# Kernel tuning notes

Hardware: AMD Instinct MI355X
Metric: run time of the kernel (lower is better)

## Reference

```python
import jax, jax.numpy as jnp
import numpy as np

B, L, D, H = 2, 1024, 1024, 16
HD = D // H
HIDDEN = 4 * D
EPS = 1e-6
SCALE = HD ** -0.5

# RoPE tables (head_dim is even, so rope_dim == head_dim)
_inv_freq = 1.0 / (10000.0 ** (np.arange(0, HD, 2, dtype=np.float32) / HD))
_freqs = np.arange(L, dtype=np.float32)[:, None] * _inv_freq[None, :]          # [L, HD/2]
COS = jnp.asarray(np.concatenate([np.cos(_freqs), np.cos(_freqs)], -1))        # [L, HD]
SIN = jnp.asarray(np.concatenate([np.sin(_freqs), np.sin(_freqs)], -1))
MASK = jnp.tril(jnp.ones((L, L), dtype=bool))                                   # causal


def _clin(xr, xi, Wr, Wi, br=None, bi=None):
    # complex linear: (a+bi)(c+di), weights stored [out, in] as in torch
    r = xr @ Wr.T - xi @ Wi.T
    i = xr @ Wi.T + xi @ Wr.T
    if br is not None:
        r = r + br
        i = i + bi
    return r, i


def _cln(xr, xi, gr, gi, br, bi):
    mr = xr.mean(-1, keepdims=True)
    mi = xi.mean(-1, keepdims=True)
    cr = xr - mr
    ci = xi - mi
    var = (cr * cr + ci * ci).mean(-1, keepdims=True)
    s = jnp.sqrt(var + EPS)
    nr = cr / s
    ni = ci / s
    return nr * gr - ni * gi + br, nr * gi + ni * gr + bi


def _rot_half(x):
    h = x.shape[-1] // 2
    return jnp.concatenate([-x[..., h:], x[..., :h]], -1)


def _rope(xr, xi):
    # apply same real rotation to real and imag parts (matches torch code)
    return (xr * COS + _rot_half(xr) * SIN, xi * COS + _rot_half(xi) * SIN)


def _split_heads(x):
    return x.reshape(B, L, H, HD).transpose(0, 2, 1, 3)  # [B,H,L,HD]


def _merge_heads(x):
    return x.transpose(0, 2, 1, 3).reshape(B, L, D)


def setup_inputs() -> dict:
    key = jax.random.key(0)
    ks = jax.random.split(key, 20)
    n = lambda k, shape, s=1.0: jax.random.normal(k, shape, dtype=jnp.float32) * s
    s_attn = (2.0 * (D + D)) ** -0.5
    s_fc1 = (2.0 * (D + HIDDEN)) ** -0.5
    s_fc2 = (2.0 * (HIDDEN + D)) ** -0.5
    return {
        'x_real': n(ks[0], (B, L, D)),
        'x_imag': n(ks[1], (B, L, D)),
        'Wq_r': n(ks[2], (D, D), s_attn), 'Wq_i': n(ks[3], (D, D), s_attn),
        'Wk_r': n(ks[4], (D, D), s_attn), 'Wk_i': n(ks[5], (D, D), s_attn),
        'Wv_r': n(ks[6], (D, D), s_attn), 'Wv_i': n(ks[7], (D, D), s_attn),
        'Wo_r': n(ks[8], (D, D), s_attn), 'Wo_i': n(ks[9], (D, D), s_attn),
        'bo_r': jnp.zeros((D,), jnp.float32), 'bo_i': jnp.zeros((D,), jnp.float32),
        'ln1_gr': jnp.ones((D,), jnp.float32), 'ln1_gi': jnp.zeros((D,), jnp.float32),
        'ln1_br': jnp.zeros((D,), jnp.float32), 'ln1_bi': jnp.zeros((D,), jnp.float32),
        'ln2_gr': jnp.ones((D,), jnp.float32), 'ln2_gi': jnp.zeros((D,), jnp.float32),
        'ln2_br': jnp.zeros((D,), jnp.float32), 'ln2_bi': jnp.zeros((D,), jnp.float32),
        'W1_r': n(ks[10], (HIDDEN, D), s_fc1), 'W1_i': n(ks[11], (HIDDEN, D), s_fc1),
        'b1_r': jnp.zeros((HIDDEN,), jnp.float32), 'b1_i': jnp.zeros((HIDDEN,), jnp.float32),
        'W2_r': n(ks[12], (D, HIDDEN), s_fc2), 'W2_i': n(ks[13], (D, HIDDEN), s_fc2),
        'b2_r': jnp.zeros((D,), jnp.float32), 'b2_i': jnp.zeros((D,), jnp.float32),
        'mod_b': n(ks[14], (HIDDEN,), 0.1),
    }


def reference(x_real, x_imag,
              Wq_r, Wq_i, Wk_r, Wk_i, Wv_r, Wv_i, Wo_r, Wo_i, bo_r, bo_i,
              ln1_gr, ln1_gi, ln1_br, ln1_bi, ln2_gr, ln2_gi, ln2_br, ln2_bi,
              W1_r, W1_i, b1_r, b1_i, W2_r, W2_i, b2_r, b2_i, mod_b):
    # --- attention sublayer (pre-LN) ---
    hr, hi = _cln(x_real, x_imag, ln1_gr, ln1_gi, ln1_br, ln1_bi)
    Qr, Qi = _clin(hr, hi, Wq_r, Wq_i)
    Kr, Ki = _clin(hr, hi, Wk_r, Wk_i)
    Vr, Vi = _clin(hr, hi, Wv_r, Wv_i)
    Qr, Qi, Kr, Ki = map(_split_heads, (Qr, Qi, Kr, Ki))
    Vr, Vi = _split_heads(Vr), _split_heads(Vi)
    Qr, Qi = _rope(Qr, Qi)
    Kr, Ki = _rope(Kr, Ki)
    # Hermitian inner product real part: Re(Q K*) = Qr.Kr + Qi.Ki
    scores = (jnp.einsum('bhld,bhmd->bhlm', Qr, Kr)
              + jnp.einsum('bhld,bhmd->bhlm', Qi, Ki)) * SCALE
    scores = jnp.where(MASK, scores, -jnp.inf)
    attn = jax.nn.softmax(scores, axis=-1)
    out_r = _merge_heads(jnp.einsum('bhlm,bhmd->bhld', attn, Vr))
    out_i = _merge_heads(jnp.einsum('bhlm,bhmd->bhld', attn, Vi))
    out_r, out_i = _clin(out_r, out_i, Wo_r, Wo_i, bo_r, bo_i)
    ar = x_real + out_r
    ai = x_imag + out_i
    # --- feed-forward sublayer (pre-LN) ---
    hr, hi = _cln(ar, ai, ln2_gr, ln2_gi, ln2_br, ln2_bi)
    fr, fi = _clin(hr, hi, W1_r, W1_i, b1_r, b1_i)
    # ModReLU: relu(|z| + b) * e^{i angle(z)}
    mag = jnp.sqrt(fr * fr + fi * fi)
    safe = jnp.where(mag > 0, mag, 1.0)
    act = jax.nn.relu(mag + mod_b)
    fr, fi = act * fr / safe, act * fi / safe
    fr, fi = _clin(fr, fi, W2_r, W2_i, b2_r, b2_i)
    return ar + fr, ai + fi
```

## Files before the change

### kernel.cpp

```cpp
#include <hip/hip_runtime.h>

#define Bq 2
#define Lq 1024
#define Dq 1024
#define Hq 16
#define HDq 64
#define HIDq 4096
#define Mq (Bq*Lq)

typedef __bf16 bf16x8 __attribute__((ext_vector_type(8)));
typedef float floatx4 __attribute__((ext_vector_type(4)));

__device__ __forceinline__ unsigned short f2us(float f){
  unsigned u = __builtin_bit_cast(unsigned, f);
  u = u + 0x7fffu + ((u >> 16) & 1u);
  return (unsigned short)(u >> 16);
}

__device__ __forceinline__ void gld16(const unsigned short* g, unsigned short* l){
  __builtin_amdgcn_global_load_lds(
      (const __attribute__((address_space(1))) unsigned int*)g,
      (__attribute__((address_space(3))) unsigned int*)l, 16, 0, 0);
}

__global__ __launch_bounds__(256) void cvt4_kernel(
    const float* __restrict__ s0, const float* __restrict__ s1,
    const float* __restrict__ s2, const float* __restrict__ s3,
    unsigned short* __restrict__ d0, unsigned short* __restrict__ d1,
    unsigned short* __restrict__ d2, unsigned short* __restrict__ d3,
    int n)
{
  const int a = blockIdx.y;
  const float* s = (a==0) ? s0 : (a==1) ? s1 : (a==2) ? s2 : s3;
  unsigned short* d = (a==0) ? d0 : (a==1) ? d1 : (a==2) ? d2 : d3;
  const int i = (blockIdx.x * 256 + threadIdx.x) * 8;
  if (i >= n) return;
  float4 v0 = ((const float4*)(s + i))[0];
  float4 v1 = ((const float4*)(s + i))[1];
  ushort4 o0, o1;
  o0.x=f2us(v0.x); o0.y=f2us(v0.y); o0.z=f2us(v0.z); o0.w=f2us(v0.w);
  o1.x=f2us(v1.x); o1.y=f2us(v1.y); o1.z=f2us(v1.z); o1.w=f2us(v1.w);
  ((ushort4*)(d + i))[0] = o0;
  ((ushort4*)(d + i))[1] = o1;
}

__global__ __launch_bounds__(256) void cln_kernel(
    const float* __restrict__ xr, const float* __restrict__ xi,
    const float* __restrict__ gr, const float* __restrict__ gi,
    const float* __restrict__ br, const float* __restrict__ bi,
    unsigned short* __restrict__ outr, unsigned short* __restrict__ outi)
{
  const int row = blockIdx.x;
  const int t = threadIdx.x;
  const int lane = t & 63, wv = t >> 6;
  __shared__ float sred[8];

  float4 v4r = ((const float4*)(xr + (size_t)row*Dq))[t];
  float4 v4i = ((const float4*)(xi + (size_t)row*Dq))[t];
  float vr[4] = {v4r.x, v4r.y, v4r.z, v4r.w};
  float vi[4] = {v4i.x, v4i.y, v4i.z, v4i.w};
  float sr = vr[0]+vr[1]+vr[2]+vr[3];
  float si = vi[0]+vi[1]+vi[2]+vi[3];
  #pragma unroll
  for (int o=32;o>0;o>>=1){ sr += __shfl_down(sr,o,64); si += __shfl_down(si,o,64); }
  if (lane==0){ sred[wv]=sr; sred[4+wv]=si; }
  __syncthreads();
  float mr = (sred[0]+sred[1]+sred[2]+sred[3]) * (1.0f/Dq);
  float mi = (sred[4]+sred[5]+sred[6]+sred[7]) * (1.0f/Dq);
  float cr[4], ci[4], vs = 0.f;
  #pragma unroll
  for (int j=0;j<4;++j){ cr[j]=vr[j]-mr; ci[j]=vi[j]-mi; vs += cr[j]*cr[j]+ci[j]*ci[j]; }
  #pragma unroll
  for (int o=32;o>0;o>>=1) vs += __shfl_down(vs,o,64);
  __syncthreads();
  if (lane==0) sred[wv]=vs;
  __syncthreads();
  float var = (sred[0]+sred[1]+sred[2]+sred[3]) * (1.0f/Dq);
  float inv = rsqrtf(var + 1e-6f);

  float4 g4r = ((const float4*)gr)[t];
  float4 g4i = ((const float4*)gi)[t];
  float4 b4r = ((const float4*)br)[t];
  float4 b4i = ((const float4*)bi)[t];
  float grf[4] = {g4r.x,g4r.y,g4r.z,g4r.w};
  float gif[4] = {g4i.x,g4i.y,g4i.z,g4i.w};
  float brf[4] = {b4r.x,b4r.y,b4r.z,b4r.w};
  float bif[4] = {b4i.x,b4i.y,b4i.z,b4i.w};
  ushort4 o_r, o_i;
  unsigned short orr[4], oii[4];
  #pragma unroll
  for (int j=0;j<4;++j){
    float nr = cr[j]*inv, ni = ci[j]*inv;
    orr[j] = f2us(nr*grf[j] - ni*gif[j] + brf[j]);
    oii[j] = f2us(nr*gif[j] + ni*grf[j] + bif[j]);
  }
  o_r.x=orr[0]; o_r.y=orr[1]; o_r.z=orr[2]; o_r.w=orr[3];
  o_i.x=oii[0]; o_i.y=oii[1]; o_i.z=oii[2]; o_i.w=oii[3];
  ((ushort4*)(outr + (size_t)row*Dq))[t] = o_r;
  ((ushort4*)(outi + (size_t)row*Dq))[t] = o_i;
}

template<int EPI, bool ROPE, bool SPLIT3>
__global__ __launch_bounds__(256,3) void cgemm16_kernel(
    const unsigned short* __restrict__ Ar, const unsigned short* __restrict__ Ai,
    const unsigned short* __restrict__ Wr, const unsigned short* __restrict__ Wi,
    void* __restrict__ Cr0, void* __restrict__ Ci0,
    void* __restrict__ Cr1, void* __restrict__ Ci1,
    void* __restrict__ Cr2, void* __restrict__ Ci2,
    const float* __restrict__ biasR, const float* __restrict__ biasI,
    const float* __restrict__ resR, const float* __restrict__ resI,
    const float* __restrict__ modb,
    int Ndim, int Kdim)
{
  const int t = threadIdx.x;
  const int w = t >> 6, lane = t & 63;
  const int quad = lane >> 4, l15 = lane & 15;
  const int wr = w >> 1, wc = w & 1;
  const int m0 = blockIdx.x * 64, n0 = blockIdx.y * 64;

  __shared__ __align__(16) unsigned short sAr0[64*32], sAi0[64*32], sWr0[64*32], sWi0[64*32];
  __shared__ __align__(16) unsigned short sAr1[64*32], sAi1[64*32], sWr1[64*32], sWi1[64*32];

  const floatx4 fz = {0.f,0.f,0.f,0.f};
  floatx4 accRR[2][2], accII[2][2], accRI[2][2], accIR[2][2];
  #pragma unroll
  for (int i=0;i<2;++i)
    #pragma unroll
    for (int j=0;j<2;++j){ accRR[i][j]=fz; accII[i][j]=fz; accRI[i][j]=fz; accIR[i][j]=fz; }

  const int srow = t >> 2;
  const int lc = ((t & 3) ^ ((t >> 2) & 3)) * 8;
  const unsigned short* pAr = Ar + (size_t)(m0 + srow)*Kdim + lc;
  const unsigned short* pAi = Ai + (size_t)(m0 + srow)*Kdim + lc;
  const unsigned short* pWr = Wr + (size_t)(n0 + srow)*Kdim + lc;
  const unsigned short* pWi = Wi + (size_t)(n0 + srow)*Kdim + lc;
  const int dst0 = t * 8;

  const int arow0 = wr*32 + l15,       arow1 = arow0 + 16;
  const int wrow0 = wc*16 + l15,       wrow1 = wrow0 + 32;
  const int aoff0 = arow0*32 + ((quad ^ (arow0 & 3))*8);
  const int aoff1 = arow1*32 + ((quad ^ (arow1 & 3))*8);
  const int woff0 = wrow0*32 + ((quad ^ (wrow0 & 3))*8);
  const int woff1 = wrow1*32 + ((quad ^ (wrow1 & 3))*8);

#define STAGEK(SA, SB, SC, SD, KOFF) do{                                   \
    gld16(pAr + (KOFF), &SA[dst0]);                                        \
    gld16(pAi + (KOFF), &SB[dst0]);                                        \
    gld16(pWr + (KOFF), &SC[dst0]);                                        \
    gld16(pWi + (KOFF), &SD[dst0]);                                        \
  }while(0)

#define COMPUTEK(SA, SB, SC, SD) do{                                       \
    bf16x8 fA0r = *(const bf16x8*)&SA[aoff0];                              \
    bf16x8 fA1r = *(const bf16x8*)&SA[aoff1];                              \
    bf16x8 fA0i = *(const bf16x8*)&SB[aoff0];                              \
    bf16x8 fA1i = *(const bf16x8*)&SB[aoff1];                              \
    bf16x8 fW0r = *(const bf16x8*)&SC[woff0];                              \
    bf16x8 fW1r = *(const bf16x8*)&SC[woff1];                              \
    bf16x8 fW0i = *(const bf16x8*)&SD[woff0];                              \
    bf16x8 fW1i = *(const bf16x8*)&SD[woff1];                              \
    accRR[0][0] = __builtin_amdgcn_mfma_f32_16x16x32_bf16(fA0r, fW0r, accRR[0][0], 0,0,0); \
    accII[0][0] = __builtin_amdgcn_mfma_f32_16x16x32_bf16(fA0i, fW0i, accII[0][0], 0,0,0); \
    accRI[0][0] = __builtin_amdgcn_mfma_f32_16x16x32_bf16(fA0r, fW0i, accRI[0][0], 0,0,0); \
    accIR[0][0] = __builtin_amdgcn_mfma_f32_16x16x32_bf16(fA0i, fW0r, accIR[0][0], 0,0,0); \
    accRR[0][1] = __builtin_amdgcn_mfma_f32_16x16x32_bf16(fA0r, fW1r, accRR[0][1], 0,0,0); \
    accII[0][1] = __builtin_amdgcn_mfma_f32_16x16x32_bf16(fA0i, fW1i, accII[0][1], 0,0,0); \
    accRI[0][1] = __builtin_amdgcn_mfma_f32_16x16x32_bf16(fA0r, fW1i, accRI[0][1], 0,0,0); \
    accIR[0][1] = __builtin_amdgcn_mfma_f32_16x16x32_bf16(fA0i, fW1r, accIR[0][1], 0,0,0); \
    accRR[1][0] = __builtin_amdgcn_mfma_f32_16x16x32_bf16(fA1r, fW0r, accRR[1][0], 0,0,0); \
    accII[1][0] = __builtin_amdgcn_mfma_f32_16x16x32_bf16(fA1i, fW0i, accII[1][0], 0,0,0); \
    accRI[1][0] = __builtin_amdgcn_mfma_f32_16x16x32_bf16(fA1r, fW0i, accRI[1][0], 0,0,0); \
    accIR[1][0] = __builtin_amdgcn_mfma_f32_16x16x32_bf16(fA1i, fW0r, accIR[1][0], 0,0,0); \
    accRR[1][1] = __builtin_amdgcn_mfma_f32_16x16x32_bf16(fA1r, fW1r, accRR[1][1], 0,0,0); \
    accII[1][1] = __builtin_amdgcn_mfma_f32_16x16x32_bf16(fA1i, fW1i, accII[1][1], 0,0,0); \
    accRI[1][1] = __builtin_amdgcn_mfma_f32_16x16x32_bf16(fA1r, fW1i, accRI[1][1], 0,0,0); \
    accIR[1][1] = __builtin_amdgcn_mfma_f32_16x16x32_bf16(fA1i, fW1r, accIR[1][1], 0,0,0); \
  }while(0)

  const int nk = Kdim >> 5;
  STAGEK(sAr0, sAi0, sWr0, sWi0, 0);
  __syncthreads();
  for (int kk=0; kk<nk; kk+=2){
    STAGEK(sAr1, sAi1, sWr1, sWi1, (size_t)(kk+1)*32);
    COMPUTEK(sAr0, sAi0, sWr0, sWi0);
    __syncthreads();
    if (kk+2 < nk) STAGEK(sAr0, sAi0, sWr0, sWi0, (size_t)(kk+2)*32);
    COMPUTEK(sAr1, sAi1, sWr1, sWi1);
    __syncthreads();
  }
#undef STAGEK
#undef COMPUTEK

  float cr[2][2][4], ci[2][2][4];
  #pragma unroll
  for (int mf=0; mf<2; ++mf)
    #pragma unroll
    for (int nf=0; nf<2; ++nf)
      #pragma unroll
      for (int r=0;r<4;++r){
        cr[mf][nf][r] = accRR[mf][nf][r] - accII[mf][nf][r];
        ci[mf][nf][r] = accRI[mf][nf][r] + accIR[mf][nf][r];
      }

  const bool doRope = ROPE && (!SPLIT3 || (n0 < 2048));
  if (doRope){
    const float invf = powf(10000.0f, -(float)(wc*16 + l15) * (1.0f/32.0f));
    #pragma unroll
    for (int mf=0; mf<2; ++mf)
      #pragma unroll
      for (int r=0;r<4;++r){
        const int gm = m0 + wr*32 + mf*16 + quad*4 + r;
        float s, c;
        sincosf((float)(gm & (Lq-1)) * invf, &s, &c);
        float xr_ = cr[mf][0][r], yr_ = cr[mf][1][r];
        cr[mf][0][r] = xr_*c - yr_*s;  cr[mf][1][r] = yr_*c + xr_*s;
        float xi_ = ci[mf][0][r], yi_ = ci[mf][1][r];
        ci[mf][0][r] = xi_*c - yi_*s;  ci[mf][1][r] = yi_*c + xi_*s;
      }
  }

  unsigned short *oR16 = nullptr, *oI16 = nullptr;
  float *oR32 = nullptr, *oI32 = nullptr;
  int ncol0, Nst;
  if (SPLIT3){
    const int aid = n0 >> 10;
    void* vr = (aid==0) ? Cr0 : ((aid==1) ? Cr1 : Cr2);
    void* vi = (aid==0) ? Ci0 : ((aid==1) ? Ci1 : Ci2);
    oR16 = (unsigned short*)vr; oI16 = (unsigned short*)vi;
    ncol0 = n0 & 1023; Nst = 1024;
  } else {
    oR16 = (unsigned short*)Cr0; oI16 = (unsigned short*)Ci0;
    oR32 = (float*)Cr0;          oI32 = (float*)Ci0;
    ncol0 = n0; Nst = Ndim;
  }

  #pragma unroll
  for (int nf=0; nf<2; ++nf){
    const int gn = n0 + wc*16 + nf*32 + l15;
    const int cn = ncol0 + wc*16 + nf*32 + l15;
    float bR = 0.f, bI = 0.f, mb = 0.f;
    if (EPI >= 1){ bR = biasR[gn]; bI = biasI[gn]; }
    if (EPI == 2){ mb = modb[gn]; }
    #pragma unroll
    for (int mf=0; mf<2; ++mf)
      #pragma unroll
      for (int r=0;r<4;++r){
        const int gm = m0 + wr*32 + mf*16 + quad*4 + r;
        const size_t idx = (size_t)gm*Nst + cn;
        float vr_ = cr[mf][nf][r] + bR, vi_ = ci[mf][nf][r] + bI;
        if (EPI == 1 || EPI == 3){ vr_ += resR[idx]; vi_ += resI[idx]; }
        if (EPI == 2){
          float mag = sqrtf(vr_*vr_ + vi_*vi_);
          float safe = (mag > 0.f) ? mag : 1.0f;
          float act = fmaxf(mag + mb, 0.f);
          float sc = act / safe;
          vr_ *= sc; vi_ *= sc;
        }
        if (EPI == 0 || EPI == 2){
          oR16[idx] = f2us(vr_);
          oI16[idx] = f2us(vi_);
        } else {
          oR32[idx] = vr_;
          oI32[idx] = vi_;
        }
      }
  }
}

__global__ __launch_bounds__(256) void vtrans_kernel(
    const unsigned short* __restrict__ Vr, const unsigned short* __restrict__ Vi,
    unsigned short* __restrict__ VTr, unsigned short* __restrict__ VTi)
{
  const int lt = blockIdx.x;
  const int bh = blockIdx.y;
  const int h = bh & (Hq-1), b = bh >> 4;
  const int t = threadIdx.x;
  __shared__ unsigned short sTr[64*65], sTi[64*65];

  const int row = t >> 2;
  const int dc  = (t & 3) * 16;
  const size_t g = ((size_t)(b*Lq) + lt*64 + row)*Dq + h*HDq + dc;
  uint4 a0 = *(const uint4*)(Vr + g);
  uint4 a1 = *(const uint4*)(Vr + g + 8);
  uint4 b0 = *(const uint4*)(Vi + g);
  uint4 b1 = *(const uint4*)(Vi + g + 8);
  const unsigned short* pa0 = (const unsigned short*)&a0;
  const unsigned short* pa1 = (const unsigned short*)&a1;
  const unsigned short* pb0 = (const unsigned short*)&b0;
  const unsigned short* pb1 = (const unsigned short*)&b1;
  #pragma unroll
  for (int e=0;e<8;++e){
    sTr[(dc+e)*65 + row]   = pa0[e];
    sTr[(dc+8+e)*65 + row] = pa1[e];
    sTi[(dc+e)*65 + row]   = pb0[e];
    sTi[(dc+8+e)*65 + row] = pb1[e];
  }
  __syncthreads();
  const int d  = t >> 2;
  const int lcx = (t & 3) * 16;
  unsigned short bufr[16], bufi[16];
  #pragma unroll
  for (int e=0;e<16;++e){
    bufr[e] = sTr[d*65 + lcx + e];
    bufi[e] = sTi[d*65 + lcx + e];
  }
  const size_t og = ((size_t)bh*HDq + d)*Lq + lt*64 + lcx;
  *(uint4*)(VTr + og)     = *(const uint4*)&bufr[0];
  *(uint4*)(VTr + og + 8) = *(const uint4*)&bufr[8];
  *(uint4*)(VTi + og)     = *(const uint4*)&bufi[0];
  *(uint4*)(VTi + og + 8) = *(const uint4*)&bufi[8];
}

__device__ __forceinline__ int swz(int v){ return v ^ ((v >> 4) & 7); }

__global__ __launch_bounds__(256,2) void fattn_kernel(
    const unsigned short* __restrict__ Qr, const unsigned short* __restrict__ Qi,
    const unsigned short* __restrict__ Kr, const unsigned short* __restrict__ Ki,
    const unsigned short* __restrict__ VTr, const unsigned short* __restrict__ VTi,
    unsigned short* __restrict__ Or, unsigned short* __restrict__ Oi)
{
  const int qt = (int)(gridDim.x - 1 - blockIdx.x);
  const int bh = blockIdx.y;
  const int h = bh & (Hq-1), b = bh >> 4;
  const int t = threadIdx.x;
  const int w = t >> 6, lane = t & 63;
  const int quad = lane >> 4, l15 = lane & 15;

  __shared__ __align__(16) unsigned short sKr[4096], sKi[4096], sVr[4096], sVi[4096];
  __shared__ __align__(16) unsigned short sP[64*72];

  const size_t qbase = ((size_t)(b*Lq) + qt*64 + w*16 + l15)*Dq + h*HDq;
  bf16x8 qr_lo = *(const bf16x8*)(Qr + qbase + quad*8);
  bf16x8 qr_hi = *(const bf16x8*)(Qr + qbase + 32 + quad*8);
  bf16x8 qi_lo = *(const bf16x8*)(Qi + qbase + quad*8);
  bf16x8 qi_hi = *(const bf16x8*)(Qi + qbase + 32 + quad*8);

  const floatx4 fzero = {0.f,0.f,0.f,0.f};
  floatx4 aOr[4], aOi[4];
  #pragma unroll
  for (int i=0;i<4;++i){ aOr[i]=fzero; aOi[i]=fzero; }
  float m_run[4] = {-1e30f,-1e30f,-1e30f,-1e30f};
  float l_run[4] = {0.f,0.f,0.f,0.f};

  const int srow = t >> 2;
  const int sns  = srow >> 4;
  const int sl15 = srow & 15;
  const int q8   = (t & 3) * 2;
  const int dstA = sns*1024 + swz(q8*16 + sl15)*8;
  const int dstB = sns*1024 + swz((q8+1)*16 + sl15)*8;

  const int rd0 = swz(quad*16 + l15)*8;
  const int rd1 = swz((4+quad)*16 + l15)*8;

  for (int kt = 0; kt <= qt; ++kt){
    const size_t kg = ((size_t)(b*Lq) + kt*64 + srow)*Dq + h*HDq + q8*8;
    uint4 ka = *(const uint4*)(Kr + kg);
    uint4 kb = *(const uint4*)(Kr + kg + 8);
    uint4 kc = *(const uint4*)(Ki + kg);
    uint4 kd = *(const uint4*)(Ki + kg + 8);
    const size_t vg = ((size_t)bh*HDq + srow)*Lq + kt*64 + q8*8;
    uint4 va = *(const uint4*)(VTr + vg);
    uint4 vb = *(const uint4*)(VTr + vg + 8);
    uint4 vc = *(const uint4*)(VTi + vg);
    uint4 vd = *(const uint4*)(VTi + vg + 8);
    __syncthreads();
    *(uint4*)&sKr[dstA] = ka;  *(uint4*)&sKr[dstB] = kb;
    *(uint4*)&sKi[dstA] = kc;  *(uint4*)&sKi[dstB] = kd;
    *(uint4*)&sVr[dstA] = va;  *(uint4*)&sVr[dstB] = vb;
    *(uint4*)&sVi[dstA] = vc;  *(uint4*)&sVi[dstB] = vd;
    __syncthreads();

    floatx4 sc[4];
    #pragma unroll
    for (int ns=0; ns<4; ++ns){
      floatx4 x = fzero;
      x = __builtin_amdgcn_mfma_f32_16x16x32_bf16(qr_lo, *(const bf16x8*)&sKr[ns*1024 + rd0], x, 0,0,0);
      x = __builtin_amdgcn_mfma_f32_16x16x32_bf16(qr_hi, *(const bf16x8*)&sKr[ns*1024 + rd1], x, 0,0,0);
      x = __builtin_amdgcn_mfma_f32_16x16x32_bf16(qi_lo, *(const bf16x8*)&sKi[ns*1024 + rd0], x, 0,0,0);
      x = __builtin_amdgcn_mfma_f32_16x16x32_bf16(qi_hi, *(const bf16x8*)&sKi[ns*1024 + rd1], x, 0,0,0);
      sc[ns] = x;
    }

    const bool diag = (kt == qt);
    float rmax[4] = {-1e30f,-1e30f,-1e30f,-1e30f};
    #pragma unroll
    for (int ns=0; ns<4; ++ns){
      #pragma unroll
      for (int r=0; r<4; ++r){
        float s = sc[ns][r] * 0.125f;
        if (diag && (ns*16 + l15 > w*16 + quad*4 + r)) s = -1e30f;
        sc[ns][r] = s;
        rmax[r] = fmaxf(rmax[r], s);
      }
    }
    #pragma unroll
    for (int off=1; off<16; off<<=1){
      #pragma unroll
      for (int r=0; r<4; ++r) rmax[r] = fmaxf(rmax[r], __shfl_xor(rmax[r], off, 64));
    }

    float alpha[4], rsum[4];
    #pragma unroll
    for (int r=0; r<4; ++r){
      float mn = fmaxf(m_run[r], rmax[r]);
      alpha[r] = __expf(m_run[r] - mn);
      m_run[r] = mn;
      rsum[r] = 0.f;
    }
    #pragma unroll
    for (int ns=0; ns<4; ++ns){
      #pragma unroll
      for (int r=0; r<4; ++r){
        float p = __expf(sc[ns][r] - m_run[r]);
        rsum[r] += p;
        sP[(w*16 + quad*4 + r)*72 + ns*16 + l15] = f2us(p);
      }
    }
    #pragma unroll
    for (int off=1; off<16; off<<=1){
      #pragma unroll
      for (int r=0; r<4; ++r) rsum[r] += __shfl_xor(rsum[r], off, 64);
    }
    #pragma unroll
    for (int r=0; r<4; ++r) l_run[r] = l_run[r]*alpha[r] + rsum[r];
    #pragma unroll
    for (int ds=0; ds<4; ++ds)
      #pragma unroll
      for (int r=0; r<4; ++r){ aOr[ds][r] *= alpha[r]; aOi[ds][r] *= alpha[r]; }

    #pragma unroll
    for (int step=0; step<2; ++step){
      bf16x8 pf = *(const bf16x8*)&sP[(w*16 + l15)*72 + step*32 + quad*8];
      const int ro = (step==0) ? rd0 : rd1;
      #pragma unroll
      for (int ds=0; ds<4; ++ds){
        aOr[ds] = __builtin_amdgcn_mfma_f32_16x16x32_bf16(pf, *(const bf16x8*)&sVr[ds*1024 + ro], aOr[ds], 0,0,0);
        aOi[ds] = __builtin_amdgcn_mfma_f32_16x16x32_bf16(pf, *(const bf16x8*)&sVi[ds*1024 + ro], aOi[ds], 0,0,0);
      }
    }
  }

  #pragma unroll
  for (int r=0; r<4; ++r){
    const float il = 1.0f / l_run[r];
    const size_t ob = ((size_t)(b*Lq) + qt*64 + w*16 + quad*4 + r)*Dq + h*HDq;
    #pragma unroll
    for (int ds=0; ds<4; ++ds){
      Or[ob + ds*16 + l15] = f2us(aOr[ds][r] * il);
      Oi[ob + ds*16 + l15] = f2us(aOi[ds][r] * il);
    }
  }
}

extern "C" void kernel_launch(void* const* d_in, const int* in_sizes, int n_in,
                              void* d_out, int out_size, void* d_ws, size_t ws_size,
                              hipStream_t stream)
{
  const float* x_r    = (const float*)d_in[0];
  const float* x_i    = (const float*)d_in[1];
  const float* Wq_r   = (const float*)d_in[2];
  const float* Wq_i   = (const float*)d_in[3];
  const float* Wk_r   = (const float*)d_in[4];
  const float* Wk_i   = (const float*)d_in[5];
  const float* Wv_r   = (const float*)d_in[6];
  const float* Wv_i   = (const float*)d_in[7];
  const float* Wo_r   = (const float*)d_in[8];
  const float* Wo_i   = (const float*)d_in[9];
  const float* bo_r   = (const float*)d_in[10];
  const float* bo_i   = (const float*)d_in[11];
  const float* ln1_gr = (const float*)d_in[12];
  const float* ln1_gi = (const float*)d_in[13];
  const float* ln1_br = (const float*)d_in[14];
  const float* ln1_bi = (const float*)d_in[15];
  const float* ln2_gr = (const float*)d_in[16];
  const float* ln2_gi = (const float*)d_in[17];
  const float* ln2_br = (const float*)d_in[18];
  const float* ln2_bi = (const float*)d_in[19];
  const float* W1_r   = (const float*)d_in[20];
  const float* W1_i   = (const float*)d_in[21];
  const float* b1_r   = (const float*)d_in[22];
  const float* b1_i   = (const float*)d_in[23];
  const float* W2_r   = (const float*)d_in[24];
  const float* W2_i   = (const float*)d_in[25];
  const float* b2_r   = (const float*)d_in[26];
  const float* b2_i   = (const float*)d_in[27];
  const float* mod_b  = (const float*)d_in[28];

  char* wsb = (char*)d_ws;
  const size_t MB = 1024*1024;
  unsigned short* bQKV_r = (unsigned short*)(wsb + 0*MB);
  unsigned short* bQKV_i = (unsigned short*)(wsb + 6*MB);
  unsigned short* bWo_r = (unsigned short*)(wsb + 12*MB);
  unsigned short* bWo_i = (unsigned short*)(wsb + 14*MB);
  unsigned short* bW1_r = (unsigned short*)(wsb + 16*MB);
  unsigned short* bW1_i = (unsigned short*)(wsb + 24*MB);
  unsigned short* bW2_r = (unsigned short*)(wsb + 32*MB);
  unsigned short* bW2_i = (unsigned short*)(wsb + 40*MB);
  unsigned short* hr  = (unsigned short*)(wsb + 48*MB);
  unsigned short* hi_ = (unsigned short*)(wsb + 52*MB);
  unsigned short* Qr  = (unsigned short*)(wsb + 56*MB);
  unsigned short* Qi  = (unsigned short*)(wsb + 60*MB);
  unsigned short* Kr  = (unsigned short*)(wsb + 64*MB);
  unsigned short* Ki  = (unsigned short*)(wsb + 68*MB);
  unsigned short* Vr  = (unsigned short*)(wsb + 72*MB);
  unsigned short* Vi  = (unsigned short*)(wsb + 76*MB);
  unsigned short* VTr = (unsigned short*)(wsb + 80*MB);
  unsigned short* VTi = (unsigned short*)(wsb + 84*MB);
  unsigned short* Or  = hr;
  unsigned short* Oi  = hi_;
  unsigned short* h2r = Qr;
  unsigned short* h2i = Qi;
  unsigned short* fr  = (unsigned short*)(wsb + 64*MB);
  unsigned short* fi  = (unsigned short*)(wsb + 80*MB);

  float* outR = (float*)d_out;
  float* outI = outR + (size_t)Mq*Dq;

  const dim3 blk(256);

  const int nDD = Dq*Dq;
  const int nDH = Dq*HIDq;
  cvt4_kernel<<<dim3(nDD/2048, 4), blk, 0, stream>>>(Wq_r, Wk_r, Wv_r, Wo_r,
      bQKV_r, bQKV_r + (size_t)nDD, bQKV_r + (size_t)2*nDD, bWo_r, nDD);
  cvt4_kernel<<<dim3(nDD/2048, 4), blk, 0, stream>>>(Wq_i, Wk_i, Wv_i, Wo_i,
      bQKV_i, bQKV_i + (size_t)nDD, bQKV_i + (size_t)2*nDD, bWo_i, nDD);
  cvt4_kernel<<<dim3(nDH/2048, 4), blk, 0, stream>>>(W1_r, W1_i, W2_r, W2_i,
      bW1_r, bW1_i, bW2_r, bW2_i, nDH);

  cln_kernel<<<Mq, blk, 0, stream>>>(x_r, x_i, ln1_gr, ln1_gi, ln1_br, ln1_bi, hr, hi_);
  cgemm16_kernel<0,true,true><<<dim3(Mq/64, 3072/64), blk, 0, stream>>>(
      hr, hi_, bQKV_r, bQKV_i,
      Qr, Qi, Kr, Ki, Vr, Vi,
      nullptr, nullptr, nullptr, nullptr, nullptr, 3072, Dq);
  vtrans_kernel<<<dim3(16, 32), blk, 0, stream>>>(Vr, Vi, VTr, VTi);
  fattn_kernel<<<dim3(16, 32), blk, 0, stream>>>(Qr, Qi, Kr, Ki, VTr, VTi, Or, Oi);
  cgemm16_kernel<1,false,false><<<dim3(Mq/64, Dq/64), blk, 0, stream>>>(
      Or, Oi, bWo_r, bWo_i, outR, outI, nullptr, nullptr, nullptr, nullptr,
      bo_r, bo_i, x_r, x_i, nullptr, Dq, Dq);
  cln_kernel<<<Mq, blk, 0, stream>>>(outR, outI, ln2_gr, ln2_gi, ln2_br, ln2_bi, h2r, h2i);
  cgemm16_kernel<2,false,false><<<dim3(Mq/64, HIDq/64), blk, 0, stream>>>(
      h2r, h2i, bW1_r, bW1_i, fr, fi, nullptr, nullptr, nullptr, nullptr,
      b1_r, b1_i, nullptr, nullptr, mod_b, HIDq, Dq);
  cgemm16_kernel<3,false,false><<<dim3(Mq/64, Dq/64), blk, 0, stream>>>(
      fr, fi, bW2_r, bW2_i, outR, outI, nullptr, nullptr, nullptr, nullptr,
      b2_r, b2_i, outR, outI, nullptr, Dq, HIDq);
}
```

Baseline: 522.4 us.

## Split-K the output-projection and FC2 complex GEMMs with a separate reduction kernel

```diff
diff --git a/kernel.cpp b/kernel.cpp
--- a/kernel.cpp
+++ b/kernel.cpp
@@ -100,7 +100,7 @@
   ((ushort4*)(outi + (size_t)row*Dq))[t] = o_i;
 }
 
-template<int EPI, bool ROPE, bool SPLIT3>
+template<int EPI, bool ROPE, bool SPLIT3, int SPLITK>
 __global__ __launch_bounds__(256,3) void cgemm16_kernel(
     const unsigned short* __restrict__ Ar, const unsigned short* __restrict__ Ai,
     const unsigned short* __restrict__ Wr, const unsigned short* __restrict__ Wi,
@@ -117,6 +117,8 @@
   const int quad = lane >> 4, l15 = lane & 15;
   const int wr = w >> 1, wc = w & 1;
   const int m0 = blockIdx.x * 64, n0 = blockIdx.y * 64;
+  const int kbase = (SPLITK > 1) ? (int)blockIdx.z * (Kdim / SPLITK) : 0;
+  const int Klen = Kdim / SPLITK;
 
   __shared__ __align__(16) unsigned short sAr0[64*32], sAi0[64*32], sWr0[64*32], sWi0[64*32];
   __shared__ __align__(16) unsigned short sAr1[64*32], sAi1[64*32], sWr1[64*32], sWi1[64*32];
@@ -130,10 +132,10 @@
 
   const int srow = t >> 2;
   const int lc = ((t & 3) ^ ((t >> 2) & 3)) * 8;
-  const unsigned short* pAr = Ar + (size_t)(m0 + srow)*Kdim + lc;
-  const unsigned short* pAi = Ai + (size_t)(m0 + srow)*Kdim + lc;
-  const unsigned short* pWr = Wr + (size_t)(n0 + srow)*Kdim + lc;
-  const unsigned short* pWi = Wi + (size_t)(n0 + srow)*Kdim + lc;
+  const unsigned short* pAr = Ar + (size_t)(m0 + srow)*Kdim + lc + kbase;
+  const unsigned short* pAi = Ai + (size_t)(m0 + srow)*Kdim + lc + kbase;
+  const unsigned short* pWr = Wr + (size_t)(n0 + srow)*Kdim + lc + kbase;
+  const unsigned short* pWi = Wi + (size_t)(n0 + srow)*Kdim + lc + kbase;
   const int dst0 = t * 8;
 
   const int arow0 = wr*32 + l15,       arow1 = arow0 + 16;
@@ -177,7 +179,7 @@
     accIR[1][1] = __builtin_amdgcn_mfma_f32_16x16x32_bf16(fA1i, fW1r, accIR[1][1], 0,0,0); \
   }while(0)
 
-  const int nk = Kdim >> 5;
+  const int nk = Klen >> 5;
   STAGEK(sAr0, sAi0, sWr0, sWi0, 0);
   __syncthreads();
   for (int kk=0; kk<nk; kk+=2){
@@ -233,13 +235,18 @@
     oR32 = (float*)Cr0;          oI32 = (float*)Ci0;
     ncol0 = n0; Nst = Ndim;
   }
+  if (EPI == 4){
+    const size_t pstride = (size_t)Mq * Ndim;
+    oR32 = (float*)Cr0 + (size_t)blockIdx.z * pstride;
+    oI32 = (float*)Ci0 + (size_t)blockIdx.z * pstride;
+  }
 
   #pragma unroll
   for (int nf=0; nf<2; ++nf){
     const int gn = n0 + wc*16 + nf*32 + l15;
     const int cn = ncol0 + wc*16 + nf*32 + l15;
     float bR = 0.f, bI = 0.f, mb = 0.f;
-    if (EPI >= 1){ bR = biasR[gn]; bI = biasI[gn]; }
+    if (EPI >= 1 && EPI <= 3){ bR = biasR[gn]; bI = biasI[gn]; }
     if (EPI == 2){ mb = modb[gn]; }
     #pragma unroll
     for (int mf=0; mf<2; ++mf)
@@ -265,6 +272,35 @@
         }
       }
   }
+}
+
+template<int NS>
+__global__ __launch_bounds__(256) void redk_kernel(
+    const float* __restrict__ pR, const float* __restrict__ pI,
+    const float* __restrict__ bR, const float* __restrict__ bI,
+    const float* __restrict__ rR, const float* __restrict__ rI,
+    float* __restrict__ oR, float* __restrict__ oI)
+{
+  const size_t MN = (size_t)Mq * Dq;
+  const size_t i = ((size_t)blockIdx.x * 256 + threadIdx.x) * 4;
+  const int col = (int)(i & (Dq - 1));
+  float4 br = *(const float4*)(bR + col);
+  float4 bi = *(const float4*)(bI + col);
+  float4 xr = *(const float4*)(rR + i);
+  float4 xi = *(const float4*)(rI + i);
+  float ar0 = br.x + xr.x, ar1 = br.y + xr.y, ar2 = br.z + xr.z, ar3 = br.w + xr.w;
+  float ai0 = bi.x + xi.x, ai1 = bi.y + xi.y, ai2 = bi.z + xi.z, ai3 = bi.w + xi.w;
+  #pragma unroll
+  for (int s=0; s<NS; ++s){
+    float4 qr = *(const float4*)(pR + s*MN + i);
+    float4 qi = *(const float4*)(pI + s*MN + i);
+    ar0 += qr.x; ar1 += qr.y; ar2 += qr.z; ar3 += qr.w;
+    ai0 += qi.x; ai1 += qi.y; ai2 += qi.z; ai3 += qi.w;
+  }
+  float4 orv = {ar0, ar1, ar2, ar3};
+  float4 oiv = {ai0, ai1, ai2, ai3};
+  *(float4*)(oR + i) = orv;
+  *(float4*)(oI + i) = oiv;
 }
 
 __global__ __launch_bounds__(256) void vtrans_kernel(
@@ -512,6 +548,9 @@
   unsigned short* h2i = Qi;
   unsigned short* fr  = (unsigned short*)(wsb + 64*MB);
   unsigned short* fi  = (unsigned short*)(wsb + 80*MB);
+  float* pR = (float*)(wsb + 96*MB);
+  float* pI = (float*)(wsb + 128*MB);
+  const bool can_split = (ws_size >= (size_t)160*MB);
 
   float* outR = (float*)d_out;
   float* outI = outR + (size_t)Mq*Dq;
@@ -528,20 +567,36 @@
       bW1_r, bW1_i, bW2_r, bW2_i, nDH);
 
   cln_kernel<<<Mq, blk, 0, stream>>>(x_r, x_i, ln1_gr, ln1_gi, ln1_br, ln1_bi, hr, hi_);
-  cgemm16_kernel<0,true,true><<<dim3(Mq/64, 3072/64), blk, 0, stream>>>(
+  cgemm16_kernel<0,true,true,1><<<dim3(Mq/64, 3072/64), blk, 0, stream>>>(
       hr, hi_, bQKV_r, bQKV_i,
       Qr, Qi, Kr, Ki, Vr, Vi,
       nullptr, nullptr, nullptr, nullptr, nullptr, 3072, Dq);
   vtrans_kernel<<<dim3(16, 32), blk, 0, stream>>>(Vr, Vi, VTr, VTi);
   fattn_kernel<<<dim3(16, 32), blk, 0, stream>>>(Qr, Qi, Kr, Ki, VTr, VTi, Or, Oi);
-  cgemm16_kernel<1,false,false><<<dim3(Mq/64, Dq/64), blk, 0, stream>>>(
-      Or, Oi, bWo_r, bWo_i, outR, outI, nullptr, nullptr, nullptr, nullptr,
-      bo_r, bo_i, x_r, x_i, nullptr, Dq, Dq);
+  if (can_split){
+    cgemm16_kernel<4,false,false,2><<<dim3(Mq/64, Dq/64, 2), blk, 0, stream>>>(
+        Or, Oi, bWo_r, bWo_i, pR, pI, nullptr, nullptr, nullptr, nullptr,
+        nullptr, nullptr, nullptr, nullptr, nullptr, Dq, Dq);
+    redk_kernel<2><<<dim3((Mq*Dq)/1024), blk, 0, stream>>>(
+        pR, pI, bo_r, bo_i, x_r, x_i, outR, outI);
+  } else {
+    cgemm16_kernel<1,false,false,1><<<dim3(Mq/64, Dq/64), blk, 0, stream>>>(
+        Or, Oi, bWo_r, bWo_i, outR, outI, nullptr, nullptr, nullptr, nullptr,
+        bo_r, bo_i, x_r, x_i, nullptr, Dq, Dq);
+  }
   cln_kernel<<<Mq, blk, 0, stream>>>(outR, outI, ln2_gr, ln2_gi, ln2_br, ln2_bi, h2r, h2i);
-  cgemm16_kernel<2,false,false><<<dim3(Mq/64, HIDq/64), blk, 0, stream>>>(
+  cgemm16_kernel<2,false,false,1><<<dim3(Mq/64, HIDq/64), blk, 0, stream>>>(
       h2r, h2i, bW1_r, bW1_i, fr, fi, nullptr, nullptr, nullptr, nullptr,
       b1_r, b1_i, nullptr, nullptr, mod_b, HIDq, Dq);
-  cgemm16_kernel<3,false,false><<<dim3(Mq/64, Dq/64), blk, 0, stream>>>(
-      fr, fi, bW2_r, bW2_i, outR, outI, nullptr, nullptr, nullptr, nullptr,
-      b2_r, b2_i, outR, outI, nullptr, Dq, HIDq);
-}
+  if (can_split){
+    cgemm16_kernel<4,false,false,4><<<dim3(Mq/64, Dq/64, 4), blk, 0, stream>>>(
+        fr, fi, bW2_r, bW2_i, pR, pI, nullptr, nullptr, nullptr, nullptr,
+        nullptr, nullptr, nullptr, nullptr, nullptr, Dq, HIDq);
+    redk_kernel<4><<<dim3((Mq*Dq)/1024), blk, 0, stream>>>(
+        pR, pI, b2_r, b2_i, outR, outI, outR, outI);
+  } else {
+    cgemm16_kernel<3,false,false,1><<<dim3(Mq/64, Dq/64), blk, 0, stream>>>(
+        fr, fi, bW2_r, bW2_i, outR, outI, nullptr, nullptr, nullptr, nullptr,
+        b2_r, b2_i, outR, outI, nullptr, Dq, HIDq);
+  }
+}
```

After: 542.7 us. +3.9%, slower.

## Triple-buffer complex GEMM LDS staging with fine-grained vmcnt waits

Applied to the files above, without the earlier changes.

```diff
diff --git a/kernel.cpp b/kernel.cpp
--- a/kernel.cpp
+++ b/kernel.cpp
@@ -118,8 +118,7 @@
   const int wr = w >> 1, wc = w & 1;
   const int m0 = blockIdx.x * 64, n0 = blockIdx.y * 64;
 
-  __shared__ __align__(16) unsigned short sAr0[64*32], sAi0[64*32], sWr0[64*32], sWi0[64*32];
-  __shared__ __align__(16) unsigned short sAr1[64*32], sAi1[64*32], sWr1[64*32], sWi1[64*32];
+  __shared__ __align__(16) unsigned short sAll[3*4*2048];
 
   const floatx4 fz = {0.f,0.f,0.f,0.f};
   floatx4 accRR[2][2], accII[2][2], accRI[2][2], accIR[2][2];
@@ -143,14 +142,18 @@
   const int woff0 = wrow0*32 + ((quad ^ (wrow0 & 3))*8);
   const int woff1 = wrow1*32 + ((quad ^ (wrow1 & 3))*8);
 
-#define STAGEK(SA, SB, SC, SD, KOFF) do{                                   \
-    gld16(pAr + (KOFF), &SA[dst0]);                                        \
-    gld16(pAi + (KOFF), &SB[dst0]);                                        \
-    gld16(pWr + (KOFF), &SC[dst0]);                                        \
-    gld16(pWi + (KOFF), &SD[dst0]);                                        \
+#define STAGEB(B, KOFF) do{                                                \
+    gld16(pAr + (KOFF), &sAll[(B)*8192 + dst0]);                           \
+    gld16(pAi + (KOFF), &sAll[(B)*8192 + 2048 + dst0]);                    \
+    gld16(pWr + (KOFF), &sAll[(B)*8192 + 4096 + dst0]);                    \
+    gld16(pWi + (KOFF), &sAll[(B)*8192 + 6144 + dst0]);                    \
   }while(0)
 
-#define COMPUTEK(SA, SB, SC, SD) do{                                       \
+#define COMPUTEB(B) do{                                                    \
+    const unsigned short* SA = &sAll[(B)*8192];                            \
+    const unsigned short* SB = SA + 2048;                                  \
+    const unsigned short* SC = SA + 4096;                                  \
+    const unsigned short* SD = SA + 6144;                                  \
     bf16x8 fA0r = *(const bf16x8*)&SA[aoff0];                              \
     bf16x8 fA1r = *(const bf16x8*)&SA[aoff1];                              \
     bf16x8 fA0i = *(const bf16x8*)&SB[aoff0];                              \
@@ -177,19 +180,31 @@
     accIR[1][1] = __builtin_amdgcn_mfma_f32_16x16x32_bf16(fA1i, fW1r, accIR[1][1], 0,0,0); \
   }while(0)
 
+#define SYNC_VM(N) do{                                                     \
+    asm volatile("s_waitcnt vmcnt(" #N ")" ::: "memory");                  \
+    __builtin_amdgcn_s_barrier();                                          \
+    asm volatile("" ::: "memory");                                         \
+  }while(0)
+#define SYNC_BAR() do{                                                     \
+    asm volatile("" ::: "memory");                                         \
+    __builtin_amdgcn_s_barrier();                                          \
+    asm volatile("" ::: "memory");                                         \
+  }while(0)
+
   const int nk = Kdim >> 5;
-  STAGEK(sAr0, sAi0, sWr0, sWi0, 0);
-  __syncthreads();
-  for (int kk=0; kk<nk; kk+=2){
-    STAGEK(sAr1, sAi1, sWr1, sWi1, (size_t)(kk+1)*32);
-    COMPUTEK(sAr0, sAi0, sWr0, sWi0);
-    __syncthreads();
-    if (kk+2 < nk) STAGEK(sAr0, sAi0, sWr0, sWi0, (size_t)(kk+2)*32);
-    COMPUTEK(sAr1, sAi1, sWr1, sWi1);
-    __syncthreads();
-  }
-#undef STAGEK
-#undef COMPUTEK
+  STAGEB(0, 0);
+  STAGEB(1, 32);
+  for (int kk=0; kk<nk-2; kk+=3){
+    STAGEB(2, (kk+2)*32);  SYNC_VM(8);  COMPUTEB(0);  SYNC_BAR();
+    STAGEB(0, (kk+3)*32);  SYNC_VM(8);  COMPUTEB(1);  SYNC_BAR();
+    STAGEB(1, (kk+4)*32);  SYNC_VM(8);  COMPUTEB(2);  SYNC_BAR();
+  }
+  SYNC_VM(4);  COMPUTEB(0);
+  SYNC_VM(0);  COMPUTEB(1);
+#undef STAGEB
+#undef COMPUTEB
+#undef SYNC_VM
+#undef SYNC_BAR
 
   float cr[2][2][4], ci[2][2][4];
   #pragma unroll
```

New measurement: 488.1 us. 1.07x faster.
